# Optimization experiments

Measured on AMD Instinct MI355X. Metric: run time of the kernel, lower is better.

## Reference

```python
import jax, jax.numpy as jnp
import numpy as np

STRIDE = 25
TOPK = 3
EPS = 1e-9


def setup_inputs() -> dict:
    key = jax.random.key(0)
    k1, k2, k3, k4 = jax.random.split(key, 4)
    B, N, T, P = 128, 200, 360, 400
    x = jax.random.normal(k1, (B, N, T), dtype=jnp.float32)
    # per-sample time-series lengths; min 100 so size_after_pool >= 1
    length = jax.random.randint(k2, (B,), 100, T + 1)
    # xavier_uniform with gain=1.414 as in nn.init.xavier_uniform_(.., gain=1.414)
    limit = float(np.sqrt(6.0 / (P + N)) * 1.414)
    patterns = jax.random.uniform(k3, (P, N), minval=-limit, maxval=limit, dtype=jnp.float32)
    # simple linear classifier standing in for Baselines.mlp(num_of_node)
    W_cls = jax.random.normal(k4, (N * N, 2), dtype=jnp.float32) * 0.01
    b_cls = jnp.zeros((2,), dtype=jnp.float32)
    return {"x": x, "length": length, "patterns": patterns, "W_cls": W_cls, "b_cls": b_cls}


def _forward(x, length, patterns, W_cls, b_cls):
    B, N, T = x.shape
    P = patterns.shape[0]
    # size_after_pool = floor(length / stride)  [B]
    sap = (length // STRIDE).astype(jnp.int32)
    # MRI_length_regularize (random_start=False): the scatter-mask keeps
    # t < size_after_pool*stride per sample; padded tail is exactly zero and
    # contributes 0 through maxpool+sum, so static full-T masking is equivalent.
    valid = (jnp.arange(T)[None, :] < (sap * STRIDE)[:, None]).astype(x.dtype)  # [B,T]
    frames = (x * valid[:, None, :]).transpose(0, 2, 1)  # [B,T,N]
    nf = frames / jnp.sqrt((frames ** 2).sum(-1, keepdims=True) + EPS)
    npat = patterns / jnp.sqrt((patterns ** 2).sum(-1, keepdims=True) + EPS)
    # top_select: keep top-K |entries| per pattern row
    _, topi = jax.lax.top_k(jnp.abs(npat), TOPK)  # [P,K]
    pmask = jnp.zeros((P, N), x.dtype).at[jnp.arange(P)[:, None], topi].set(1.0)
    toppattern = pmask * npat
    # scores + strided max-pool over time
    scores = jnp.einsum('btn,pn->bpt', nf, npat)  # [B,P,T]
    nwin = T // STRIDE
    pos = scores[:, :, : nwin * STRIDE].reshape(B, P, nwin, STRIDE).max(-1)  # [B,P,nwin]
    finalscore = (pos / sap[:, None, None].astype(x.dtype)).sum(-1)  # [B,P]
    # realpattern = toppattern.detach(); graphs = R^T diag(finalscore) R / (maskgraph+eps)
    realpattern = jax.lax.stop_gradient(toppattern)
    maskgraph = pmask.T @ pmask  # [N,N]
    graphs = jnp.einsum('pn,bp,pm->bnm', realpattern, finalscore, realpattern) / (maskgraph + EPS)
    out = graphs.reshape(B, -1) @ W_cls + b_cls  # [B,2]
    # Critical_ROI(normalized_patterns, toppattern)
    norm = (((1.0 - jnp.linalg.norm(toppattern, axis=-1) / jnp.linalg.norm(npat, axis=-1)) ** 2).sum() / 800.0)
    rec = jnp.zeros((1,), x.dtype)
    return out, norm, rec


def reference(x, length, patterns, W_cls, b_cls):
    return _forward(x, length, patterns, W_cls, b_cls)
```

## Files before the change

kernel.cpp:

```cpp
#include <hip/hip_runtime.h>

#define N_NODE 200
#define T_LEN 360
#define T_POOL 350
#define T_PAD 384
#define P_PAT 400
#define P_PAD 512
#define NWIN 14
#define STRIDE_ 25
#define KPAD 224

#define O_AH    0
#define O_XT    229376
#define O_INVN  22249472
#define O_POS   22446080
#define O_TOPN  26116096
#define O_TOPV  26120896
#define O_NORMT 26125696

typedef unsigned short u16;
typedef __attribute__((ext_vector_type(8))) short bf16x8;
typedef __attribute__((ext_vector_type(4))) float f32x4;

__device__ __forceinline__ unsigned fkey(float f) {
    unsigned u = __float_as_uint(f);
    return (u & 0x80000000u) ? ~u : (u | 0x80000000u);
}
__device__ __forceinline__ u16 f2bf(float f) {
    unsigned u = __float_as_uint(f);
    unsigned r = u + 0x7FFFu + ((u >> 16) & 1u);
    return (u16)(r >> 16);
}

__global__ __launch_bounds__(256) void k_prep(
    const float* __restrict__ x, const int* __restrict__ length,
    const float* __restrict__ pat,
    u16* __restrict__ Ah, u16* __restrict__ XT, float* __restrict__ invn,
    int* __restrict__ topn_w, float* __restrict__ topv_w, float* __restrict__ normt,
    unsigned* __restrict__ pos)
{
    __shared__ unsigned ldsw[2176];
    int blk = blockIdx.x, tid = threadIdx.x;

    {
        int base = blk * 256 + tid;
        #pragma unroll
        for (int i = 0; i < 7; ++i) pos[base + i * 131072] = 0u;
    }

    if (blk < 128) {
        int lane = tid & 63;
        int p = blk * 4 + (tid >> 6);
        bool pv = p < P_PAT;
        float sv[4], av[4];
        int nn[4];
        float ss = 0.f;
        #pragma unroll
        for (int j = 0; j < 4; ++j) {
            int n = lane + 64 * j;
            nn[j] = n;
            if (pv && n < N_NODE) { float v = pat[p * N_NODE + n]; sv[j] = v; av[j] = fabsf(v); ss += v * v; }
            else { sv[j] = 0.f; av[j] = -1.f; }
        }
        #pragma unroll
        for (int off = 32; off >= 1; off >>= 1) ss += __shfl_xor(ss, off);
        float rn = 1.0f / sqrtf(ss + 1e-9f);

        int pb = p >> 6, ii = (p >> 4) & 3, plm = p & 15;
        #pragma unroll
        for (int j = 0; j < 4; ++j) {
            int n = nn[j];
            if (n < KPAD) {
                float v = (pv && n < N_NODE) ? sv[j] * rn : 0.f;
                int s = n >> 5, c = n & 31, quad = c >> 3, e = c & 7;
                size_t idx = ((size_t)((s * 8 + pb) * 4 + ii) * 64 + quad * 16 + plm) * 8 + e;
                Ah[idx] = f2bf(v);
            }
        }
        if (!pv) return;

        int topn[3]; float topv[3];
        for (int r = 0; r < 3; ++r) {
            float bv = -2.f; int bi = 1 << 30;
            #pragma unroll
            for (int j = 0; j < 4; ++j)
                if (av[j] > bv || (av[j] == bv && nn[j] < bi)) { bv = av[j]; bi = nn[j]; }
            #pragma unroll
            for (int off = 32; off >= 1; off >>= 1) {
                float ov = __shfl_xor(bv, off); int oi = __shfl_xor(bi, off);
                if (ov > bv || (ov == bv && oi < bi)) { bv = ov; bi = oi; }
            }
            int jj = bi >> 6, src = bi & 63;
            float rawj = (jj == 0) ? sv[0] : (jj == 1) ? sv[1] : (jj == 2) ? sv[2] : sv[3];
            float raw = __shfl(rawj, src);
            topn[r] = bi; topv[r] = raw * rn;
            #pragma unroll
            for (int j = 0; j < 4; ++j) if (nn[j] == bi) av[j] = -1.f;
        }
        float fullnorm = sqrtf(ss) * rn;
        float topnorm = sqrtf(topv[0]*topv[0] + topv[1]*topv[1] + topv[2]*topv[2]);
        if (lane == 0) {
            float d = 1.0f - topnorm / fullnorm;
            normt[p] = d * d * (1.0f / 800.0f);
        }
        if (lane < 3) { topn_w[p * 3 + lane] = topn[lane]; topv_w[p * 3 + lane] = topv[lane]; }
        return;
    }

    int b1 = blk - 128;
    int b = b1 / 3, ti = b1 - 3 * b;
    int t0 = ti * 128;
    int th = tid & 127, cg = tid >> 7;
    int t = t0 + th;
    bool tok = t < T_LEN;
    const float* xb = x + (size_t)b * (N_NODE * T_LEN);
    float ssq = 0.f;

    int t2 = tid & 127, qh = tid >> 7;
    int tbw = (t0 + t2) >> 6;
    int jjw = (t2 >> 4) & 3;
    int lmw = t2 & 15;

    for (int c = 0; c < 7; ++c) {
        int k0 = c * 32;
        #pragma unroll
        for (int cc8 = 0; cc8 < 8; ++cc8) {
            int cc = cg * 8 + cc8;
            int k = k0 + cc * 2;
            float v0 = (tok && k     < N_NODE) ? xb[k * T_LEN + t]       : 0.f;
            float v1 = (tok && k + 1 < N_NODE) ? xb[(k + 1) * T_LEN + t] : 0.f;
            ssq = fmaf(v0, v0, fmaf(v1, v1, ssq));
            ldsw[th * 17 + cc] = (unsigned)f2bf(v0) | ((unsigned)f2bf(v1) << 16);
        }
        __syncthreads();
        {
            size_t rowbase = (size_t)(b * 6 + tbw) * 14336 + (size_t)(c * 4 + jjw) * 512 + lmw * 8;
            #pragma unroll
            for (int u = 0; u < 2; ++u) {
                int q = qh + 2 * u;
                uint4 val = make_uint4(ldsw[t2 * 17 + q * 4 + 0], ldsw[t2 * 17 + q * 4 + 1],
                                       ldsw[t2 * 17 + q * 4 + 2], ldsw[t2 * 17 + q * 4 + 3]);
                *(uint4*)&XT[rowbase + q * 128] = val;
            }
        }
        __syncthreads();
    }
    ((float*)ldsw)[tid] = ssq;
    __syncthreads();
    if (tid < 128) {
        float tot = ((float*)ldsw)[tid] + ((float*)ldsw)[tid + 128];
        int sap = length[b] / STRIDE_;
        int tvalid = sap * STRIDE_;
        float iv = (t0 + tid < tvalid) ? 1.0f / (sqrtf(tot + 1e-9f) * (float)sap) : 0.f;
        invn[b * T_PAD + t0 + tid] = iv;
    }
}

__global__ __launch_bounds__(256, 2) void k_mm(
    const u16* __restrict__ Ah, const u16* __restrict__ XT,
    const float* __restrict__ invn, unsigned* __restrict__ pos)
{
    __shared__ __align__(16) float Ss[16 * 132];
    int tid = threadIdx.x, blk = blockIdx.x;
    int xcd = blk & 7, slot = blk >> 3;
    int g = slot / 12, r = slot - 12 * g;
    int b = xcd + 8 * g;
    int t0 = (r % 3) * 128;
    int p0 = (r / 3) * 128;
    int lane = tid & 63, wid = tid >> 6;
    int quad = lane >> 4, lm = lane & 15;
    int wp = wid >> 1, wt = wid & 1;
    int pbq = (p0 >> 6) + wp;
    int tb = (t0 >> 6) + wt;

    const u16* Ab = Ah + (size_t)pbq * 2048 + lane * 8;
    const u16* Xb = XT + (size_t)(b * 6 + tb) * 14336 + lane * 8;

    f32x4 acc[4][4];
    #pragma unroll
    for (int i = 0; i < 4; ++i)
        #pragma unroll
        for (int j = 0; j < 4; ++j) acc[i][j] = (f32x4){0.f, 0.f, 0.f, 0.f};

    auto LA = [&](bf16x8* d, int s) {
        const u16* p = Ab + (size_t)s * 16384;
        #pragma unroll
        for (int i = 0; i < 4; ++i) d[i] = *(const bf16x8*)(p + i * 512);
    };
    auto MM = [&](bf16x8* a, bf16x8* xv) {
        #pragma unroll
        for (int i = 0; i < 4; ++i)
            #pragma unroll
            for (int j = 0; j < 4; ++j)
                acc[i][j] = __builtin_amdgcn_mfma_f32_16x16x32_bf16(a[i], xv[j], acc[i][j], 0, 0, 0);
    };

    bf16x8 a0[4], a1[4], xf[16], xg[12];
    LA(a0, 0);
    #pragma unroll
    for (int s = 0; s < 4; ++s)
        #pragma unroll
        for (int j = 0; j < 4; ++j) xf[s * 4 + j] = *(const bf16x8*)(Xb + (s * 4 + j) * 512);
    LA(a1, 1);
    MM(a0, &xf[0]);
    LA(a0, 2);
    MM(a1, &xf[4]);
    #pragma unroll
    for (int s = 4; s < 7; ++s)
        #pragma unroll
        for (int j = 0; j < 4; ++j) xg[(s - 4) * 4 + j] = *(const bf16x8*)(Xb + (s * 4 + j) * 512);
    LA(a1, 3);
    MM(a0, &xf[8]);
    LA(a0, 4);
    MM(a1, &xf[12]);
    LA(a1, 5);
    MM(a0, &xg[0]);
    LA(a0, 6);
    MM(a1, &xg[4]);
    MM(a0, &xg[8]);

    float invv[4];
    #pragma unroll
    for (int j = 0; j < 4; ++j) invv[j] = invn[b * T_PAD + t0 + wt * 64 + j * 16 + lm];

    int wbase = t0 / STRIDE_;
    int tmax = min(t0 + 128, T_POOL);
    for (int rr = 0; rr < 4; ++rr) {
        __syncthreads();
        if (wp == (rr >> 1)) {
            #pragma unroll
            for (int i2 = 0; i2 < 2; ++i2) {
                int i = (rr & 1) * 2 + i2;
                #pragma unroll
                for (int j = 0; j < 4; ++j) {
                    int col = wt * 64 + j * 16 + lm;
                    #pragma unroll
                    for (int q = 0; q < 4; ++q)
                        Ss[(i2 * 16 + quad * 4 + q) * 132 + col] = acc[i][j][q] * invv[j];
                }
            }
        }
        __syncthreads();
        int sidx = tid & 7, pl = tid >> 3;
        int w = wbase + sidx;
        int tlo = max(w * STRIDE_, t0), thi = min(w * STRIDE_ + STRIDE_, tmax);
        if (w < NWIN && tlo < thi) {
            float m = -3.4e38f;
            for (int t = tlo; t < thi; ++t) m = fmaxf(m, Ss[pl * 132 + (t - t0)]);
            atomicMax(&pos[((size_t)b * P_PAD + p0 + rr * 32 + pl) * NWIN + w], fkey(m));
        }
    }
}

__global__ void k_out(const unsigned* __restrict__ pos, const int* __restrict__ topn_w,
                      const float* __restrict__ topv_w, const float* __restrict__ W,
                      const float* __restrict__ normt, const float* __restrict__ bcls,
                      float* __restrict__ out)
{
    __shared__ unsigned maskT[N_NODE * 13];
    __shared__ float cf0[P_PAT], cf1[P_PAT];
    __shared__ float sh[512];
    int b = blockIdx.x, tid = threadIdx.x;

    for (int i = tid; i < N_NODE * 13; i += 256) maskT[i] = 0u;
    __syncthreads();
    for (int idx = tid; idx < P_PAT * 3; idx += 256) {
        int q = idx / 3;
        int n = topn_w[idx];
        atomicOr(&maskT[n * 13 + (q >> 5)], 1u << (q & 31));
    }
    __syncthreads();

    for (int p = tid; p < P_PAT; p += 256) {
        int tn[3]; float tv[3];
        #pragma unroll
        for (int i = 0; i < 3; ++i) { tn[i] = topn_w[p * 3 + i]; tv[i] = topv_w[p * 3 + i]; }
        float c0 = 0.f, c1 = 0.f;
        #pragma unroll
        for (int i = 0; i < 3; ++i)
            #pragma unroll
            for (int j = 0; j < 3; ++j) {
                int a = tn[i], bb = tn[j];
                int mgv = 0;
                #pragma unroll
                for (int w = 0; w < 13; ++w)
                    mgv += __popc(maskT[a * 13 + w] & maskT[bb * 13 + w]);
                int nm = a * N_NODE + bb;
                float f = tv[i] * tv[j] / ((float)mgv + 1e-9f);
                c0 += f * W[nm * 2 + 0];
                c1 += f * W[nm * 2 + 1];
            }
        cf0[p] = c0; cf1[p] = c1;
    }
    __syncthreads();
    float s0 = 0.f, s1 = 0.f;
    for (int p = tid; p < P_PAT; p += 256) {
        const unsigned* pp = pos + ((size_t)b * P_PAD + p) * NWIN;
        float fs = 0.f;
        #pragma unroll
        for (int w = 0; w < NWIN; ++w) {
            unsigned k = pp[w];
            unsigned u = (k & 0x80000000u) ? (k ^ 0x80000000u) : ~k;
            fs += __uint_as_float(u);
        }
        s0 += fs * cf0[p];
        s1 += fs * cf1[p];
    }
    sh[tid] = s0; sh[256 + tid] = s1;
    __syncthreads();
    for (int o = 128; o > 0; o >>= 1) {
        if (tid < o) { sh[tid] += sh[tid + o]; sh[256 + tid] += sh[256 + tid + o]; }
        __syncthreads();
    }
    if (tid == 0) {
        out[b * 2 + 0] = sh[0]   + bcls[0];
        out[b * 2 + 1] = sh[256] + bcls[1];
    }
    if (b == 0) {
        __syncthreads();
        float ns = 0.f;
        for (int i = tid; i < P_PAT; i += 256) ns += normt[i];
        sh[tid] = ns;
        __syncthreads();
        for (int o = 128; o > 0; o >>= 1) {
            if (tid < o) sh[tid] += sh[tid + o];
            __syncthreads();
        }
        if (tid == 0) { out[256] = sh[0]; out[257] = 0.f; }
    }
}

extern "C" void kernel_launch(void* const* d_in, const int* in_sizes, int n_in,
                              void* d_out, int out_size, void* d_ws, size_t ws_size,
                              hipStream_t stream) {
    (void)in_sizes; (void)n_in; (void)out_size; (void)ws_size;
    const float* x        = (const float*)d_in[0];
    const int*   length   = (const int*)d_in[1];
    const float* patterns = (const float*)d_in[2];
    const float* Wcls     = (const float*)d_in[3];
    const float* bcls     = (const float*)d_in[4];
    float* out = (float*)d_out;
    char* ws = (char*)d_ws;

    u16*      Ah    = (u16*)(ws + O_AH);
    u16*      XT    = (u16*)(ws + O_XT);
    float*    invn  = (float*)(ws + O_INVN);
    unsigned* pos   = (unsigned*)(ws + O_POS);
    int*      topn  = (int*)(ws + O_TOPN);
    float*    topv  = (float*)(ws + O_TOPV);
    float*    normt = (float*)(ws + O_NORMT);

    k_prep<<<512, 256, 0, stream>>>(x, length, patterns, Ah, XT, invn,
                                    topn, topv, normt, pos);
    k_mm<<<1536, 256, 0, stream>>>(Ah, XT, invn, pos);
    k_out<<<128, 256, 0, stream>>>(pos, topn, topv, Wcls, normt, bcls, out);
}
```

Baseline: 136.6 us.

## Split prep transpose by node chunk and defer norm reduction to matmul

The x-transpose/bf16 conversion in k_prep now runs one block per (batch, 32-node chunk) instead of one per (batch, 128-time tile) looping over seven chunks. This gives 1024 blocks with a single LDS barrier each rather than 384 blocks with fourteen barriers. Per-chunk partial sums of squares go to a workspace buffer. k_mm then sums the seven partials and applies the length mask and 1/sap scaling itself, which adds a few extra global reads per thread there.

```diff
diff --git a/kernel.cpp b/kernel.cpp
--- a/kernel.cpp
+++ b/kernel.cpp
@@ -12,11 +12,11 @@
 
 #define O_AH    0
 #define O_XT    229376
-#define O_INVN  22249472
-#define O_POS   22446080
-#define O_TOPN  26116096
-#define O_TOPV  26120896
-#define O_NORMT 26125696
+#define O_SSQP  22249472
+#define O_POS   23625728
+#define O_TOPN  27295744
+#define O_TOPV  27300544
+#define O_NORMT 27305344
 
 typedef unsigned short u16;
 typedef __attribute__((ext_vector_type(8))) short bf16x8;
@@ -33,19 +33,21 @@
 }
 
 __global__ __launch_bounds__(256) void k_prep(
-    const float* __restrict__ x, const int* __restrict__ length,
-    const float* __restrict__ pat,
-    u16* __restrict__ Ah, u16* __restrict__ XT, float* __restrict__ invn,
+    const float* __restrict__ x, const float* __restrict__ pat,
+    u16* __restrict__ Ah, u16* __restrict__ XT, float* __restrict__ ssqp,
     int* __restrict__ topn_w, float* __restrict__ topv_w, float* __restrict__ normt,
     unsigned* __restrict__ pos)
 {
-    __shared__ unsigned ldsw[2176];
+    __shared__ unsigned ldsw[16 * 388];
     int blk = blockIdx.x, tid = threadIdx.x;
 
     {
-        int base = blk * 256 + tid;
-        #pragma unroll
-        for (int i = 0; i < 7; ++i) pos[base + i * 131072] = 0u;
+        int idx = blk * 256 + tid;
+        #pragma unroll
+        for (int i = 0; i < 4; ++i) {
+            int w = idx + i * 262144;
+            if (w < 917504) pos[w] = 0u;
+        }
     }
 
     if (blk < 128) {
@@ -107,58 +109,50 @@
         return;
     }
 
-    int b1 = blk - 128;
-    int b = b1 / 3, ti = b1 - 3 * b;
-    int t0 = ti * 128;
-    int th = tid & 127, cg = tid >> 7;
-    int t = t0 + th;
-    bool tok = t < T_LEN;
+    int bc = blk - 128;
+    int b = bc / 7, c = bc - 7 * b;
+    int k0 = c * 32;
     const float* xb = x + (size_t)b * (N_NODE * T_LEN);
-    float ssq = 0.f;
-
-    int t2 = tid & 127, qh = tid >> 7;
-    int tbw = (t0 + t2) >> 6;
-    int jjw = (t2 >> 4) & 3;
-    int lmw = t2 & 15;
-
-    for (int c = 0; c < 7; ++c) {
-        int k0 = c * 32;
-        #pragma unroll
-        for (int cc8 = 0; cc8 < 8; ++cc8) {
-            int cc = cg * 8 + cc8;
-            int k = k0 + cc * 2;
-            float v0 = (tok && k     < N_NODE) ? xb[k * T_LEN + t]       : 0.f;
-            float v1 = (tok && k + 1 < N_NODE) ? xb[(k + 1) * T_LEN + t] : 0.f;
-            ssq = fmaf(v0, v0, fmaf(v1, v1, ssq));
-            ldsw[th * 17 + cc] = (unsigned)f2bf(v0) | ((unsigned)f2bf(v1) << 16);
-        }
-        __syncthreads();
-        {
-            size_t rowbase = (size_t)(b * 6 + tbw) * 14336 + (size_t)(c * 4 + jjw) * 512 + lmw * 8;
-            #pragma unroll
-            for (int u = 0; u < 2; ++u) {
-                int q = qh + 2 * u;
-                uint4 val = make_uint4(ldsw[t2 * 17 + q * 4 + 0], ldsw[t2 * 17 + q * 4 + 1],
-                                       ldsw[t2 * 17 + q * 4 + 2], ldsw[t2 * 17 + q * 4 + 3]);
-                *(uint4*)&XT[rowbase + q * 128] = val;
-            }
-        }
-        __syncthreads();
-    }
-    ((float*)ldsw)[tid] = ssq;
-    __syncthreads();
-    if (tid < 128) {
-        float tot = ((float*)ldsw)[tid] + ((float*)ldsw)[tid + 128];
-        int sap = length[b] / STRIDE_;
-        int tvalid = sap * STRIDE_;
-        float iv = (t0 + tid < tvalid) ? 1.0f / (sqrtf(tot + 1e-9f) * (float)sap) : 0.f;
-        invn[b * T_PAD + t0 + tid] = iv;
+    bool tok2 = tid < (T_LEN - 256);
+    float ssq0 = 0.f, ssq1 = 0.f;
+
+    #pragma unroll
+    for (int kkp = 0; kkp < 16; ++kkp) {
+        int k = k0 + 2 * kkp;
+        bool kv0 = k < N_NODE, kv1 = (k + 1) < N_NODE;
+        float v0 = kv0 ? xb[k * T_LEN + tid]             : 0.f;
+        float v1 = kv1 ? xb[(k + 1) * T_LEN + tid]       : 0.f;
+        float w0 = (kv0 && tok2) ? xb[k * T_LEN + 256 + tid]       : 0.f;
+        float w1 = (kv1 && tok2) ? xb[(k + 1) * T_LEN + 256 + tid] : 0.f;
+        ssq0 = fmaf(v0, v0, fmaf(v1, v1, ssq0));
+        ssq1 = fmaf(w0, w0, fmaf(w1, w1, ssq1));
+        ldsw[kkp * 388 + tid] = (unsigned)f2bf(v0) | ((unsigned)f2bf(v1) << 16);
+        if (tid < 128)
+            ldsw[kkp * 388 + 256 + tid] = (unsigned)f2bf(w0) | ((unsigned)f2bf(w1) << 16);
+    }
+    ssqp[(size_t)(b * 7 + c) * 384 + tid] = ssq0;
+    if (tid < 128) ssqp[(size_t)(b * 7 + c) * 384 + 256 + tid] = ssq1;
+    __syncthreads();
+
+    #pragma unroll
+    for (int i = 0; i < 6; ++i) {
+        int u = i * 256 + tid;
+        int lm = u & 15, q = (u >> 4) & 3, j = (u >> 6) & 3, tb = u >> 8;
+        int t = tb * 64 + j * 16 + lm;
+        uint4 val;
+        if (t < T_LEN)
+            val = make_uint4(ldsw[(q * 4 + 0) * 388 + t], ldsw[(q * 4 + 1) * 388 + t],
+                             ldsw[(q * 4 + 2) * 388 + t], ldsw[(q * 4 + 3) * 388 + t]);
+        else
+            val = make_uint4(0u, 0u, 0u, 0u);
+        *(uint4*)&XT[(size_t)(b * 6 + tb) * 14336 + (size_t)(c * 4 + j) * 512 + q * 128 + lm * 8] = val;
     }
 }
 
 __global__ __launch_bounds__(256, 2) void k_mm(
     const u16* __restrict__ Ah, const u16* __restrict__ XT,
-    const float* __restrict__ invn, unsigned* __restrict__ pos)
+    const float* __restrict__ ssqp, const int* __restrict__ length,
+    unsigned* __restrict__ pos)
 {
     __shared__ __align__(16) float Ss[16 * 132];
     int tid = threadIdx.x, blk = blockIdx.x;
@@ -219,9 +213,17 @@
     MM(a1, &xg[4]);
     MM(a0, &xg[8]);
 
+    int sap = length[b] / STRIDE_;
+    int tvalid = sap * STRIDE_;
     float invv[4];
     #pragma unroll
-    for (int j = 0; j < 4; ++j) invv[j] = invn[b * T_PAD + t0 + wt * 64 + j * 16 + lm];
+    for (int j = 0; j < 4; ++j) {
+        int t = t0 + wt * 64 + j * 16 + lm;
+        float tot = 0.f;
+        #pragma unroll
+        for (int c = 0; c < 7; ++c) tot += ssqp[(size_t)(b * 7 + c) * 384 + t];
+        invv[j] = (t < tvalid) ? 1.0f / (sqrtf(tot + 1e-9f) * (float)sap) : 0.f;
+    }
 
     int wbase = t0 / STRIDE_;
     int tmax = min(t0 + 128, T_POOL);
@@ -344,14 +346,14 @@
 
     u16*      Ah    = (u16*)(ws + O_AH);
     u16*      XT    = (u16*)(ws + O_XT);
-    float*    invn  = (float*)(ws + O_INVN);
+    float*    ssqp  = (float*)(ws + O_SSQP);
     unsigned* pos   = (unsigned*)(ws + O_POS);
     int*      topn  = (int*)(ws + O_TOPN);
     float*    topv  = (float*)(ws + O_TOPV);
     float*    normt = (float*)(ws + O_NORMT);
 
-    k_prep<<<512, 256, 0, stream>>>(x, length, patterns, Ah, XT, invn,
-                                    topn, topv, normt, pos);
-    k_mm<<<1536, 256, 0, stream>>>(Ah, XT, invn, pos);
+    k_prep<<<1024, 256, 0, stream>>>(x, patterns, Ah, XT, ssqp,
+                                     topn, topv, normt, pos);
+    k_mm<<<1536, 256, 0, stream>>>(Ah, XT, ssqp, length, pos);
     k_out<<<128, 256, 0, stream>>>(pos, topn, topv, Wcls, normt, bcls, out);
 }
```

After: 127.0 us. 1.08x faster.
